# Kernel optimization log

Hardware: AMD Instinct MI355X
Metric: run time of the kernel (lower is better)

The kernel has to match this reference:

```python
import jax, jax.numpy as jnp
import numpy as np

N = 50000   # nodes
R = 4       # relation groups
E = 800000  # nnz per relation adjacency
ED = 200000 # decoded edges
H = 128     # hidden_dim
L = 64      # latent_dim
DH = 64     # decoder_hidden_dim


def setup_inputs() -> dict:
    key = jax.random.key(0)
    ks = iter(jax.random.split(key, 64))
    def nrm(shape, scale=1.0):
        return jax.random.normal(next(ks), shape, dtype=jnp.float32) * scale
    inp = {}
    inp["x_process"] = nrm((N, 62))
    inp["x_file"] = nrm((N, 37))
    inp["x_network"] = nrm((N, 37))
    def lin(prefix, din, dout):
        s = 1.0 / np.sqrt(din)
        inp[prefix + "_Ws"] = nrm((dout, din), s)
        inp[prefix + "_bs"] = nrm((dout,), s)
        inp[prefix + "_Wr"] = nrm((R, dout, din), s)
        inp[prefix + "_br"] = nrm((R, dout), s)
    lin("p1", 62, H); lin("p2", H, L)
    lin("f1", 37, H); lin("f2", H, L)
    lin("n1", 37, H); lin("n2", H, L)
    inp["gate_W"] = nrm((3, L), 1.0 / np.sqrt(L))
    inp["gate_b"] = nrm((3,), 0.1)
    inp["dec_W1"] = nrm((DH, 4 * L), 1.0 / np.sqrt(4 * L))
    inp["dec_b1"] = nrm((DH,), 0.1)
    inp["dec_W2"] = nrm((1, DH), 1.0 / np.sqrt(DH))
    inp["dec_b2"] = nrm((1,), 0.1)
    inp["adj_rows"] = jax.random.randint(next(ks), (R, E), 0, N, dtype=jnp.int32)
    inp["adj_cols"] = jax.random.randint(next(ks), (R, E), 0, N, dtype=jnp.int32)
    inp["adj_vals"] = jax.random.uniform(next(ks), (R, E), dtype=jnp.float32) * 0.1
    inp["edge_src"] = jax.random.randint(next(ks), (ED,), 0, N, dtype=jnp.int32)
    inp["edge_dst"] = jax.random.randint(next(ks), (ED,), 0, N, dtype=jnp.int32)
    return inp


def reference(x_process, x_file, x_network,
              p1_Ws, p1_bs, p1_Wr, p1_br, p2_Ws, p2_bs, p2_Wr, p2_br,
              f1_Ws, f1_bs, f1_Wr, f1_br, f2_Ws, f2_bs, f2_Wr, f2_br,
              n1_Ws, n1_bs, n1_Wr, n1_br, n2_Ws, n2_bs, n2_Wr, n2_br,
              gate_W, gate_b, dec_W1, dec_b1, dec_W2, dec_b2,
              adj_rows, adj_cols, adj_vals, edge_src, edge_dst):
    def spmm(rows, cols, vals, x):  # A @ x, A in COO: out[row] += val * x[col]
        return jax.ops.segment_sum(vals[:, None] * x[cols], rows, num_segments=N)

    def rgcn_layer(x, Ws, bs, Wr, br):
        out = x @ Ws.T + bs  # self_linear
        for r in range(R):
            out = out + spmm(adj_rows[r], adj_cols[r], adj_vals[r], x) @ Wr[r].T + br[r]
        return out / float(R + 1)

    def encoder(x, W1s, b1s, W1r, b1r, W2s, b2s, W2r, b2r):
        h = jax.nn.relu(rgcn_layer(x, W1s, b1s, W1r, b1r))
        # dropout p=0.0 / eval mode -> identity
        return rgcn_layer(h, W2s, b2s, W2r, b2r)

    z_p = encoder(x_process, p1_Ws, p1_bs, p1_Wr, p1_br, p2_Ws, p2_bs, p2_Wr, p2_br)
    z_f = encoder(x_file, f1_Ws, f1_bs, f1_Wr, f1_br, f2_Ws, f2_bs, f2_Wr, f2_br)
    z_n = encoder(x_network, n1_Ws, n1_bs, n1_Wr, n1_br, n2_Ws, n2_bs, n2_Wr, n2_br)

    # gated multi-view fusion: three Linear(latent,1) gates -> softmax over views
    scores = jnp.stack([z_p @ gate_W[0] + gate_b[0],
                        z_f @ gate_W[1] + gate_b[1],
                        z_n @ gate_W[2] + gate_b[2]], axis=1)  # [N, 3]
    alpha = jax.nn.softmax(scores, axis=1)
    z = alpha[:, 0:1] * z_p + alpha[:, 1:2] * z_f + alpha[:, 2:3] * z_n  # [N, L]

    # mlp edge decoder
    zs = z[edge_src]
    zd = z[edge_dst]
    feats = jnp.concatenate([zs, zd, zs * zd, jnp.abs(zs - zd)], axis=1)  # [ED, 4L]
    hid = jax.nn.relu(feats @ dec_W1.T + dec_b1)
    logits = (hid @ dec_W2.T + dec_b2)[:, 0]  # [ED]
    return logits
```

## Files before the change

### kernel.cpp

```cpp
#include <hip/hip_runtime.h>

#define N_NODES 50000
#define R_REL   4
#define E_NNZ   800000
#define ED_EDGES 200000
#define H_DIM   128
#define L_DIM   64

#define RN_TOTAL (R_REL * N_NODES)
#define ETOT     (R_REL * E_NNZ)

#define EPB   8192
#define NB    391
#define RBK   196
#define KBK   (R_REL * RBK)
#define HTOT  (KBK * NB)
#define SCB   300
#define MAXB  6144

#define WS_RP    0u
#define WS_HIST  800256u
#define WS_BSUM  2026496u
#define WS_BIAS3 2028544u
#define WS_CV    2030592u
#define WS_YALL  27630720u
#define WS_TMP   27630720u
#define WS_SF    53230720u
#define WS_SN    82830720u
#define WS_XALL  112430720u
#define WS_YSP   112430720u
#define WS_SP    131630720u
#define WS_HF    131630720u
#define WS_YSN   131630720u
#define WS_HN    157230720u
#define WS_HPR   188001536u
#define WS_YSF   188001536u
#define WS_Z     200801536u

__device__ __forceinline__ ushort f2bf(float f) {
    unsigned u = __float_as_uint(f);
    unsigned r = (u + 0x7fffu + ((u >> 16) & 1u)) >> 16;
    return (ushort)r;
}
__device__ __forceinline__ float bf2f(ushort u) {
    return __uint_as_float(((unsigned)u) << 16);
}

__global__ void cast_xall_kernel(const float* __restrict__ xp, const float* __restrict__ xf,
                                 const float* __restrict__ xn, ushort* __restrict__ xall) {
    int i = blockIdx.x * 256 + threadIdx.x;
    if (i >= N_NODES * 192) return;
    int node = i / 192, k = i - node * 192;
    float v = 0.f;
    if (k < 62) v = xp[node * 62 + k];
    else if (k >= 64 && k < 138) {
        int j = k - 64, d = j >> 1;
        v = (j & 1) ? xn[node * 37 + d] : xf[node * 37 + d];
    }
    xall[i] = f2bf(v);
}

__global__ void radix_hist_kernel(const int* __restrict__ rows, int* __restrict__ H) {
    __shared__ int hist[KBK];
    int blk = blockIdx.x, t = threadIdx.x;
    for (int i = t; i < KBK; i += 256) hist[i] = 0;
    __syncthreads();
    int base = blk * EPB;
    #pragma unroll 1
    for (int i = 0; i < EPB / 256; i++) {
        int g = base + i * 256 + t;
        if (g < ETOT) {
            int r = g / E_NNZ;
            atomicAdd(&hist[r * RBK + (rows[g] >> 8)], 1);
        }
    }
    __syncthreads();
    for (int i = t; i < KBK; i += 256) H[i * NB + blk] = hist[i];
}

__global__ void scan_part_kernel(const int* __restrict__ H, int* __restrict__ bsum) {
    __shared__ int red[256];
    int base = blockIdx.x * 1024, t = threadIdx.x;
    int s = 0;
    #pragma unroll
    for (int i = 0; i < 4; i++) {
        int idx = base + i * 256 + t;
        if (idx < HTOT) s += H[idx];
    }
    red[t] = s; __syncthreads();
    for (int d = 128; d > 0; d >>= 1) {
        if (t < d) red[t] += red[t + d];
        __syncthreads();
    }
    if (t == 0) bsum[blockIdx.x] = red[0];
}

__global__ void scan_bsum_kernel(int* __restrict__ bsum, int* __restrict__ rp) {
    __shared__ int sh[512];
    int t = threadIdx.x;
    int v = (t < SCB) ? bsum[t] : 0;
    sh[t] = v; __syncthreads();
    for (int d = 1; d < 512; d <<= 1) {
        int u = (t >= d) ? sh[t - d] : 0;
        __syncthreads();
        sh[t] += u;
        __syncthreads();
    }
    if (t < SCB) bsum[t] = sh[t] - v;
    if (t == 0) rp[RN_TOTAL] = ETOT;
}

__global__ void scan_final_kernel(int* __restrict__ H, const int* __restrict__ bsum) {
    __shared__ int sh[256];
    int base = blockIdx.x * 1024, t = threadIdx.x;
    int c[4]; int s = 0;
    #pragma unroll
    for (int i = 0; i < 4; i++) {
        int idx = base + t * 4 + i;
        c[i] = (idx < HTOT) ? H[idx] : 0;
        s += c[i];
    }
    sh[t] = s; __syncthreads();
    for (int d = 1; d < 256; d <<= 1) {
        int u = (t >= d) ? sh[t - d] : 0;
        __syncthreads();
        sh[t] += u;
        __syncthreads();
    }
    int off = bsum[blockIdx.x] + sh[t] - s;
    #pragma unroll
    for (int i = 0; i < 4; i++) {
        int idx = base + t * 4 + i;
        if (idx < HTOT) H[idx] = off;
        off += c[i];
    }
}

__global__ void radix_scatter_kernel(const int* __restrict__ rows, const int* __restrict__ cols,
                                     const float* __restrict__ vals, const int* __restrict__ H,
                                     int2* __restrict__ tmp) {
    __shared__ int cur[KBK];
    int blk = blockIdx.x, t = threadIdx.x;
    for (int i = t; i < KBK; i += 256) cur[i] = H[i * NB + blk];
    __syncthreads();
    int base = blk * EPB;
    #pragma unroll 1
    for (int i = 0; i < EPB / 256; i++) {
        int g = base + i * 256 + t;
        if (g < ETOT) {
            int r = g / E_NNZ;
            int row = rows[g];
            int b = r * RBK + (row >> 8);
            int p = atomicAdd(&cur[b], 1);
            tmp[p] = make_int2(cols[g] | ((row & 255) << 16), __float_as_int(vals[g]));
        }
    }
}

__launch_bounds__(256)
__global__ void bucket_sort_kernel(const int2* __restrict__ tmp, const int* __restrict__ H,
                                   int* __restrict__ rp, int2* __restrict__ cse) {
    __shared__ int hist[256];
    __shared__ int sc[256];
    __shared__ int cur[256];
    __shared__ int2 eb[MAXB];
    int b = blockIdx.x, t = threadIdx.x;
    int start = H[b * NB];
    int end = (b == KBK - 1) ? ETOT : H[(b + 1) * NB];
    int cnt = end - start;
    bool useLds = (cnt <= MAXB);
    hist[t] = 0;
    __syncthreads();
    for (int i = t; i < cnt; i += 256) {
        int2 e = tmp[start + i];
        if (useLds) eb[i] = e;
        atomicAdd(&hist[(e.x >> 16) & 255], 1);
    }
    __syncthreads();
    sc[t] = hist[t]; __syncthreads();
    for (int d = 1; d < 256; d <<= 1) {
        int v = (t >= d) ? sc[t - d] : 0;
        __syncthreads();
        sc[t] += v;
        __syncthreads();
    }
    int pref = sc[t] - hist[t];
    int r = b / RBK, rh = b - r * RBK;
    int grow = rh * 256 + t;
    if (grow < N_NODES) rp[r * N_NODES + grow] = start + pref;
    cur[t] = start + pref;
    __syncthreads();
    for (int i = t; i < cnt; i += 256) {
        int2 e = useLds ? eb[i] : tmp[start + i];
        int rl = (e.x >> 16) & 255;
        int p = atomicAdd(&cur[rl], 1);
        cse[p] = make_int2(e.x & 0xFFFF, e.y);
    }
}

__global__ void spmm1_all_kernel(const ushort* __restrict__ xall,
                                 const int* __restrict__ rp, const int2* __restrict__ cse,
                                 float* __restrict__ Sp, float* __restrict__ Sf,
                                 float* __restrict__ Sn) {
    int wave = threadIdx.x >> 6, lane = threadIdx.x & 63;
    int row = blockIdx.x * 4 + wave;
    if (row >= N_NODES) return;
    int h = lane >> 5, j = lane & 31;
    unsigned d0 = 2u * (unsigned)j;
    unsigned po = d0;
    unsigned fo = 64u + 2u * d0;
    for (int r = 0; r < R_REL; r++) {
        int e0 = rp[r * N_NODES + row], e1 = rp[r * N_NODES + row + 1];
        float ap0 = 0.f, ap1 = 0.f, af0 = 0.f, af1 = 0.f, an0 = 0.f, an1 = 0.f;
        int e = e0;
        for (; e + 8 <= e1; e += 8) {
            int2 qA = cse[e + h],     qB = cse[e + 2 + h];
            int2 qC = cse[e + 4 + h], qD = cse[e + 6 + h];
            unsigned bA = (unsigned)qA.x * 192u, bB = (unsigned)qB.x * 192u;
            unsigned bC = (unsigned)qC.x * 192u, bD = (unsigned)qD.x * 192u;
            ushort2 pA = *(const ushort2*)(xall + bA + po);
            ushort2 pB = *(const ushort2*)(xall + bB + po);
            ushort2 pC = *(const ushort2*)(xall + bC + po);
            ushort2 pD = *(const ushort2*)(xall + bD + po);
            ushort4 uA = *(const ushort4*)(xall + bA + fo);
            ushort4 uB = *(const ushort4*)(xall + bB + fo);
            ushort4 uC = *(const ushort4*)(xall + bC + fo);
            ushort4 uD = *(const ushort4*)(xall + bD + fo);
            float vA = __int_as_float(qA.y), vB = __int_as_float(qB.y);
            float vC = __int_as_float(qC.y), vD = __int_as_float(qD.y);
            ap0 += vA * bf2f(pA.x) + vB * bf2f(pB.x) + vC * bf2f(pC.x) + vD * bf2f(pD.x);
            ap1 += vA * bf2f(pA.y) + vB * bf2f(pB.y) + vC * bf2f(pC.y) + vD * bf2f(pD.y);
            af0 += vA * bf2f(uA.x) + vB * bf2f(uB.x) + vC * bf2f(uC.x) + vD * bf2f(uD.x);
            an0 += vA * bf2f(uA.y) + vB * bf2f(uB.y) + vC * bf2f(uC.y) + vD * bf2f(uD.y);
            af1 += vA * bf2f(uA.z) + vB * bf2f(uB.z) + vC * bf2f(uC.z) + vD * bf2f(uD.z);
            an1 += vA * bf2f(uA.w) + vB * bf2f(uB.w) + vC * bf2f(uC.w) + vD * bf2f(uD.w);
        }
        for (; e < e1; e += 2) {
            int idx = e + h;
            int2 q = cse[idx < e1 ? idx : e1 - 1];
            float v = (idx < e1) ? __int_as_float(q.y) : 0.f;
            unsigned b = (unsigned)q.x * 192u;
            ushort2 p = *(const ushort2*)(xall + b + po);
            ushort4 u = *(const ushort4*)(xall + b + fo);
            ap0 += v * bf2f(p.x); ap1 += v * bf2f(p.y);
            af0 += v * bf2f(u.x); an0 += v * bf2f(u.y);
            af1 += v * bf2f(u.z); an1 += v * bf2f(u.w);
        }
        ap0 += __shfl_xor(ap0, 32); ap1 += __shfl_xor(ap1, 32);
        af0 += __shfl_xor(af0, 32); af1 += __shfl_xor(af1, 32);
        an0 += __shfl_xor(an0, 32); an1 += __shfl_xor(an1, 32);
        if (h == 0) {
            int d = (int)d0;
            if (d < 62) *(float2*)(Sp + row * 248 + r * 62 + d) = make_float2(ap0, ap1);
            float* sfp = Sf + row * 148 + r * 37;
            float* snp = Sn + row * 148 + r * 37;
            if (d < 37) { sfp[d] = af0; snp[d] = an0; }
            if (d < 36) { sfp[d + 1] = af1; snp[d + 1] = an1; }
        }
    }
}

__launch_bounds__(256)
__global__ void gemm1_kernel(const float* __restrict__ x, const float* __restrict__ S,
                             const float* __restrict__ Ws, const float* __restrict__ bs,
                             const float* __restrict__ Wr, const float* __restrict__ br,
                             float* __restrict__ h, int din) {
    __shared__ float sA[64 * 63];
    __shared__ float sW[62 * 132];
    int t = threadIdx.x;
    int i0 = blockIdx.x * 64;
    int rg = t >> 5, cg = t & 31;
    float acc[8][4] = {};
    for (int s = 0; s < 5; s++) {
        const float* Aptr; int astride;
        if (s == 0) { Aptr = x; astride = din; }
        else        { Aptr = S + (s - 1) * din; astride = 4 * din; }
        const float* Wp = (s == 0) ? Ws : (Wr + (s - 1) * H_DIM * din);
        __syncthreads();
        for (int idx = t; idx < 64 * din; idx += 256) {
            int rr = idx / din, k = idx - rr * din;
            int grow = i0 + rr;
            sA[rr * 63 + k] = (grow < N_NODES) ? Aptr[grow * astride + k] : 0.f;
        }
        for (int idx = t; idx < H_DIM * din; idx += 256) {
            int j = idx / din, k = idx - j * din;
            sW[k * 132 + j] = Wp[j * din + k];
        }
        __syncthreads();
        for (int k = 0; k < din; k++) {
            float a[8];
            #pragma unroll
            for (int rr = 0; rr < 8; rr++) a[rr] = sA[(rg * 8 + rr) * 63 + k];
            float4 w = *(const float4*)&sW[k * 132 + cg * 4];
            #pragma unroll
            for (int rr = 0; rr < 8; rr++) {
                acc[rr][0] += a[rr] * w.x; acc[rr][1] += a[rr] * w.y;
                acc[rr][2] += a[rr] * w.z; acc[rr][3] += a[rr] * w.w;
            }
        }
    }
    int j0 = cg * 4;
    float btot[4];
    #pragma unroll
    for (int cc = 0; cc < 4; cc++) {
        float b = bs[j0 + cc];
        #pragma unroll
        for (int r = 0; r < R_REL; r++) b += br[r * H_DIM + j0 + cc];
        btot[cc] = b;
    }
    #pragma unroll
    for (int rr = 0; rr < 8; rr++) {
        int grow = i0 + rg * 8 + rr;
        if (grow < N_NODES) {
            float4 o;
            o.x = fmaxf((acc[rr][0] + btot[0]) * 0.2f, 0.f);
            o.y = fmaxf((acc[rr][1] + btot[1]) * 0.2f, 0.f);
            o.z = fmaxf((acc[rr][2] + btot[2]) * 0.2f, 0.f);
            o.w = fmaxf((acc[rr][3] + btot[3]) * 0.2f, 0.f);
            *(float4*)&h[grow * H_DIM + j0] = o;
        }
    }
}

__launch_bounds__(256)
__global__ void gemm2_kernel(const float* __restrict__ h, const float* __restrict__ Ws2,
                             const float* __restrict__ Wr2, float* __restrict__ Yself,
                             ushort* __restrict__ Yall, int view) {
    __shared__ float sA[128 * 65];
    __shared__ float sW[64 * 68];
    int t = threadIdx.x;
    int i0 = blockIdx.x * 128;
    int ct = blockIdx.y;
    int rg = t >> 4, cg = t & 15;
    const float* Wp = (ct == 0) ? Ws2 : (Wr2 + (ct - 1) * 64 * H_DIM);
    float acc[8][4] = {};
    for (int kc = 0; kc < 2; kc++) {
        __syncthreads();
        for (int idx = t; idx < 128 * 64; idx += 256) {
            int rr = idx >> 6, k = idx & 63;
            int grow = i0 + rr;
            sA[rr * 65 + k] = (grow < N_NODES) ? h[grow * H_DIM + kc * 64 + k] : 0.f;
        }
        for (int idx = t; idx < 64 * 64; idx += 256) {
            int j = idx >> 6, k = idx & 63;
            sW[k * 68 + j] = Wp[j * H_DIM + kc * 64 + k];
        }
        __syncthreads();
        for (int k = 0; k < 64; k++) {
            float a[8];
            #pragma unroll
            for (int rr = 0; rr < 8; rr++) a[rr] = sA[(rg * 8 + rr) * 65 + k];
            float4 w = *(const float4*)&sW[k * 68 + cg * 4];
            #pragma unroll
            for (int rr = 0; rr < 8; rr++) {
                acc[rr][0] += a[rr] * w.x; acc[rr][1] += a[rr] * w.y;
                acc[rr][2] += a[rr] * w.z; acc[rr][3] += a[rr] * w.w;
            }
        }
    }
    #pragma unroll
    for (int rr = 0; rr < 8; rr++) {
        int grow = i0 + rg * 8 + rr;
        if (grow < N_NODES) {
            if (ct == 0) {
                float4 o = make_float4(acc[rr][0], acc[rr][1], acc[rr][2], acc[rr][3]);
                *(float4*)&Yself[(size_t)grow * 64 + cg * 4] = o;
            } else {
                ushort4 o;
                o.x = f2bf(acc[rr][0]); o.y = f2bf(acc[rr][1]);
                o.z = f2bf(acc[rr][2]); o.w = f2bf(acc[rr][3]);
                *(ushort4*)&Yall[(size_t)grow * 768 + (ct - 1) * 192 + view * 64 + cg * 4] = o;
            }
        }
    }
}

__global__ void bias_prep_kernel(const float* __restrict__ pbs, const float* __restrict__ pbr,
                                 const float* __restrict__ fbs, const float* __restrict__ fbr,
                                 const float* __restrict__ nbs, const float* __restrict__ nbr,
                                 float* __restrict__ bias3) {
    int t = threadIdx.x;
    if (t >= 192) return;
    int view = t >> 6, d = t & 63;
    const float* bs = (view == 0) ? pbs : (view == 1) ? fbs : nbs;
    const float* br = (view == 0) ? pbr : (view == 1) ? fbr : nbr;
    float b = bs[d];
    #pragma unroll
    for (int r = 0; r < R_REL; r++) b += br[r * 64 + d];
    bias3[t] = b;
}

__launch_bounds__(256)
__global__ void spmm2z_all_kernel(const float* __restrict__ Ysp,
                                  const float* __restrict__ Ysf,
                                  const float* __restrict__ Ysn,
                                  const ushort* __restrict__ Yall,
                                  const int* __restrict__ rp, const int2* __restrict__ cse,
                                  const float* __restrict__ bias3,
                                  const float* __restrict__ gW, const float* __restrict__ gb,
                                  float* __restrict__ z) {
    int wave = threadIdx.x >> 6, lane = threadIdx.x & 63;
    int row = blockIdx.x * 4 + wave;
    if (row >= N_NODES) return;
    int h = lane >> 5, j = lane & 31;
    unsigned d0 = 2u * (unsigned)j;
    float aP0 = 0.f, aP1 = 0.f, aF0 = 0.f, aF1 = 0.f, aN0 = 0.f, aN1 = 0.f;
    for (int r = 0; r < R_REL; r++) {
        int e0 = rp[r * N_NODES + row], e1 = rp[r * N_NODES + row + 1];
        unsigned ofs = (unsigned)(r * 192) + d0;
        int e = e0;
        for (; e + 8 <= e1; e += 8) {
            int2 qA = cse[e + h],     qB = cse[e + 2 + h];
            int2 qC = cse[e + 4 + h], qD = cse[e + 6 + h];
            unsigned oA = (unsigned)qA.x * 768u + ofs;
            unsigned oB = (unsigned)qB.x * 768u + ofs;
            unsigned oC = (unsigned)qC.x * 768u + ofs;
            unsigned oD = (unsigned)qD.x * 768u + ofs;
            ushort2 pA = *(const ushort2*)(Yall + oA);
            ushort2 fA = *(const ushort2*)(Yall + oA + 64);
            ushort2 nA = *(const ushort2*)(Yall + oA + 128);
            ushort2 pB = *(const ushort2*)(Yall + oB);
            ushort2 fB = *(const ushort2*)(Yall + oB + 64);
            ushort2 nB = *(const ushort2*)(Yall + oB + 128);
            ushort2 pC = *(const ushort2*)(Yall + oC);
            ushort2 fC = *(const ushort2*)(Yall + oC + 64);
            ushort2 nC = *(const ushort2*)(Yall + oC + 128);
            ushort2 pD = *(const ushort2*)(Yall + oD);
            ushort2 fD = *(const ushort2*)(Yall + oD + 64);
            ushort2 nD = *(const ushort2*)(Yall + oD + 128);
            float vA = __int_as_float(qA.y), vB = __int_as_float(qB.y);
            float vC = __int_as_float(qC.y), vD = __int_as_float(qD.y);
            aP0 += vA * bf2f(pA.x) + vB * bf2f(pB.x) + vC * bf2f(pC.x) + vD * bf2f(pD.x);
            aP1 += vA * bf2f(pA.y) + vB * bf2f(pB.y) + vC * bf2f(pC.y) + vD * bf2f(pD.y);
            aF0 += vA * bf2f(fA.x) + vB * bf2f(fB.x) + vC * bf2f(fC.x) + vD * bf2f(fD.x);
            aF1 += vA * bf2f(fA.y) + vB * bf2f(fB.y) + vC * bf2f(fC.y) + vD * bf2f(fD.y);
            aN0 += vA * bf2f(nA.x) + vB * bf2f(nB.x) + vC * bf2f(nC.x) + vD * bf2f(nD.x);
            aN1 += vA * bf2f(nA.y) + vB * bf2f(nB.y) + vC * bf2f(nC.y) + vD * bf2f(nD.y);
        }
        for (; e < e1; e += 2) {
            int idx = e + h;
            int2 q = cse[idx < e1 ? idx : e1 - 1];
            float v = (idx < e1) ? __int_as_float(q.y) : 0.f;
            unsigned o = (unsigned)q.x * 768u + ofs;
            ushort2 p = *(const ushort2*)(Yall + o);
            ushort2 f = *(const ushort2*)(Yall + o + 64);
            ushort2 n = *(const ushort2*)(Yall + o + 128);
            aP0 += v * bf2f(p.x); aP1 += v * bf2f(p.y);
            aF0 += v * bf2f(f.x); aF1 += v * bf2f(f.y);
            aN0 += v * bf2f(n.x); aN1 += v * bf2f(n.y);
        }
    }
    aP0 += __shfl_xor(aP0, 32); aP1 += __shfl_xor(aP1, 32);
    aF0 += __shfl_xor(aF0, 32); aF1 += __shfl_xor(aF1, 32);
    aN0 += __shfl_xor(aN0, 32); aN1 += __shfl_xor(aN1, 32);
    size_t rb = (size_t)row * 64 + d0;
    float2 ysp = *(const float2*)(Ysp + rb);
    float2 ysf = *(const float2*)(Ysf + rb);
    float2 ysn = *(const float2*)(Ysn + rb);
    aP0 = (aP0 + ysp.x + bias3[d0]) * 0.2f;
    aP1 = (aP1 + ysp.y + bias3[d0 + 1]) * 0.2f;
    aF0 = (aF0 + ysf.x + bias3[64 + d0]) * 0.2f;
    aF1 = (aF1 + ysf.y + bias3[64 + d0 + 1]) * 0.2f;
    aN0 = (aN0 + ysn.x + bias3[128 + d0]) * 0.2f;
    aN1 = (aN1 + ysn.y + bias3[128 + d0 + 1]) * 0.2f;
    float sp = aP0 * gW[d0] + aP1 * gW[d0 + 1];
    float sf = aF0 * gW[64 + d0] + aF1 * gW[64 + d0 + 1];
    float sn = aN0 * gW[128 + d0] + aN1 * gW[128 + d0 + 1];
    #pragma unroll
    for (int d = 16; d >= 1; d >>= 1) {
        sp += __shfl_xor(sp, d);
        sf += __shfl_xor(sf, d);
        sn += __shfl_xor(sn, d);
    }
    sp += gb[0]; sf += gb[1]; sn += gb[2];
    float m = fmaxf(sp, fmaxf(sf, sn));
    float ep = __expf(sp - m), ef = __expf(sf - m), en = __expf(sn - m);
    float inv = 1.f / (ep + ef + en);
    if (h == 0) {
        float2 zo;
        zo.x = (ep * aP0 + ef * aF0 + en * aN0) * inv;
        zo.y = (ep * aP1 + ef * aF1 + en * aN1) * inv;
        *(float2*)(z + rb) = zo;
    }
}

__launch_bounds__(512)
__global__ void decoder6_kernel(const float* __restrict__ z, const int* __restrict__ esrc,
                                const int* __restrict__ edst, const float* __restrict__ w1,
                                const float* __restrict__ b1, const float* __restrict__ w2,
                                const float* __restrict__ b2, float* __restrict__ out) {
    __shared__ float sW1[16384];
    int t = threadIdx.x;
    for (int i = t; i < 4096; i += 512)
        ((float4*)sW1)[i] = ((const float4*)w1)[i];
    __syncthreads();
    int e = blockIdx.x * 512 + t;
    if (e >= ED_EDGES) return;
    int s = esrc[e], d = edst[e];
    const float4* zs = (const float4*)(z + (size_t)s * 64);
    const float4* zd = (const float4*)(z + (size_t)d * 64);
    float hid[64];
    #pragma unroll
    for (int j = 0; j < 64; j++) hid[j] = 0.f;
    #pragma unroll 1
    for (int kc = 0; kc < 16; kc++) {
        float4 a = zs[kc], b = zd[kc];
        float4 p, q;
        p.x = a.x * b.x; q.x = fabsf(a.x - b.x);
        p.y = a.y * b.y; q.y = fabsf(a.y - b.y);
        p.z = a.z * b.z; q.z = fabsf(a.z - b.z);
        p.w = a.w * b.w; q.w = fabsf(a.w - b.w);
        const float* wb0 = sW1 + kc * 4;
        #pragma unroll
        for (int j = 0; j < 64; j++) {
            const float* wr = wb0 + j * 256;
            float4 wa = *(const float4*)(wr);
            float4 wbv = *(const float4*)(wr + 64);
            float4 wc = *(const float4*)(wr + 128);
            float4 wd = *(const float4*)(wr + 192);
            hid[j] += a.x * wa.x + a.y * wa.y + a.z * wa.z + a.w * wa.w
                    + b.x * wbv.x + b.y * wbv.y + b.z * wbv.z + b.w * wbv.w
                    + p.x * wc.x + p.y * wc.y + p.z * wc.z + p.w * wc.w
                    + q.x * wd.x + q.y * wd.y + q.z * wd.z + q.w * wd.w;
        }
    }
    float lg = b2[0];
    #pragma unroll
    for (int j = 0; j < 64; j++)
        lg += fmaxf(hid[j] + b1[j], 0.f) * w2[j];
    out[e] = lg;
}

extern "C" void kernel_launch(void* const* d_in, const int* in_sizes, int n_in,
                              void* d_out, int out_size, void* d_ws, size_t ws_size,
                              hipStream_t stream) {
    const float* x_p = (const float*)d_in[0];
    const float* x_f = (const float*)d_in[1];
    const float* x_n = (const float*)d_in[2];
    const float* p1_Ws = (const float*)d_in[3];  const float* p1_bs = (const float*)d_in[4];
    const float* p1_Wr = (const float*)d_in[5];  const float* p1_br = (const float*)d_in[6];
    const float* p2_Ws = (const float*)d_in[7];  const float* p2_bs = (const float*)d_in[8];
    const float* p2_Wr = (const float*)d_in[9];  const float* p2_br = (const float*)d_in[10];
    const float* f1_Ws = (const float*)d_in[11]; const float* f1_bs = (const float*)d_in[12];
    const float* f1_Wr = (const float*)d_in[13]; const float* f1_br = (const float*)d_in[14];
    const float* f2_Ws = (const float*)d_in[15]; const float* f2_bs = (const float*)d_in[16];
    const float* f2_Wr = (const float*)d_in[17]; const float* f2_br = (const float*)d_in[18];
    const float* n1_Ws = (const float*)d_in[19]; const float* n1_bs = (const float*)d_in[20];
    const float* n1_Wr = (const float*)d_in[21]; const float* n1_br = (const float*)d_in[22];
    const float* n2_Ws = (const float*)d_in[23]; const float* n2_bs = (const float*)d_in[24];
    const float* n2_Wr = (const float*)d_in[25]; const float* n2_br = (const float*)d_in[26];
    const float* gate_W = (const float*)d_in[27]; const float* gate_b = (const float*)d_in[28];
    const float* dec_W1 = (const float*)d_in[29]; const float* dec_b1 = (const float*)d_in[30];
    const float* dec_W2 = (const float*)d_in[31]; const float* dec_b2 = (const float*)d_in[32];
    const int*   adj_rows = (const int*)d_in[33];
    const int*   adj_cols = (const int*)d_in[34];
    const float* adj_vals = (const float*)d_in[35];
    const int*   edge_src = (const int*)d_in[36];
    const int*   edge_dst = (const int*)d_in[37];

    char* ws = (char*)d_ws;
    int*    rp   = (int*)(ws + WS_RP);
    int*    H    = (int*)(ws + WS_HIST);
    int*    bsum = (int*)(ws + WS_BSUM);
    float*  bias3 = (float*)(ws + WS_BIAS3);
    int2*   cse  = (int2*)(ws + WS_CV);
    int2*   tmp  = (int2*)(ws + WS_TMP);
    ushort* xall = (ushort*)(ws + WS_XALL);
    ushort* Yall = (ushort*)(ws + WS_YALL);
    float*  S_p = (float*)(ws + WS_SP);
    float*  S_f = (float*)(ws + WS_SF);
    float*  S_n = (float*)(ws + WS_SN);
    float*  h_p = (float*)(ws + WS_HPR);
    float*  h_f = (float*)(ws + WS_HF);
    float*  h_n = (float*)(ws + WS_HN);
    float*  Ys_p = (float*)(ws + WS_YSP);
    float*  Ys_f = (float*)(ws + WS_YSF);
    float*  Ys_n = (float*)(ws + WS_YSN);
    float*  z    = (float*)(ws + WS_Z);
    float*  out  = (float*)d_out;

    cast_xall_kernel<<<(N_NODES * 192 + 255) / 256, 256, 0, stream>>>(x_p, x_f, x_n, xall);

    radix_hist_kernel<<<NB, 256, 0, stream>>>(adj_rows, H);
    scan_part_kernel<<<SCB, 256, 0, stream>>>(H, bsum);
    scan_bsum_kernel<<<1, 512, 0, stream>>>(bsum, rp);
    scan_final_kernel<<<SCB, 256, 0, stream>>>(H, bsum);
    radix_scatter_kernel<<<NB, 256, 0, stream>>>(adj_rows, adj_cols, adj_vals, H, tmp);
    bucket_sort_kernel<<<KBK, 256, 0, stream>>>(tmp, H, rp, cse);

    spmm1_all_kernel<<<N_NODES / 4, 256, 0, stream>>>(xall, rp, cse, S_p, S_f, S_n);

    int g1 = (N_NODES + 63) / 64;
    gemm1_kernel<<<g1, 256, 0, stream>>>(x_p, S_p, p1_Ws, p1_bs, p1_Wr, p1_br, h_p, 62);
    gemm1_kernel<<<g1, 256, 0, stream>>>(x_f, S_f, f1_Ws, f1_bs, f1_Wr, f1_br, h_f, 37);
    gemm1_kernel<<<g1, 256, 0, stream>>>(x_n, S_n, n1_Ws, n1_bs, n1_Wr, n1_br, h_n, 37);

    dim3 g2((N_NODES + 127) / 128, 5);
    gemm2_kernel<<<g2, 256, 0, stream>>>(h_p, p2_Ws, p2_Wr, Ys_p, Yall, 0);
    gemm2_kernel<<<g2, 256, 0, stream>>>(h_f, f2_Ws, f2_Wr, Ys_f, Yall, 1);
    gemm2_kernel<<<g2, 256, 0, stream>>>(h_n, n2_Ws, n2_Wr, Ys_n, Yall, 2);

    bias_prep_kernel<<<1, 192, 0, stream>>>(p2_bs, p2_br, f2_bs, f2_br, n2_bs, n2_br, bias3);
    spmm2z_all_kernel<<<N_NODES / 4, 256, 0, stream>>>(
        Ys_p, Ys_f, Ys_n, Yall, rp, cse, bias3, gate_W, gate_b, z);

    decoder6_kernel<<<(ED_EDGES + 511) / 512, 512, 0, stream>>>(
        z, edge_src, edge_dst, dec_W1, dec_b1, dec_W2, dec_b2, out);
}
```

Before: 1.436 ms.

## Split decoder hidden units across blocks and process two edges per thread

The decoder now splits the 64 hidden units into two halves along a second grid dimension. Each block stages only half of W1 in LDS (32 KB instead of 64 KB), and each thread computes two edges so every LDS weight load is reused twice. Per-half partial logits go to a workspace buffer and a new combine kernel sums them and adds the output bias. The intent is to cut LDS traffic per FLOP and raise occupancy. In exchange it adds an extra launch, a partial-sum round trip through global memory, and each z row is gathered twice (once per half).

```diff
diff --git a/kernel.cpp b/kernel.cpp
--- a/kernel.cpp
+++ b/kernel.cpp
@@ -25,6 +25,7 @@
 #define WS_CV    2030592u
 #define WS_YALL  27630720u
 #define WS_TMP   27630720u
+#define WS_PART  27630720u
 #define WS_SF    53230720u
 #define WS_SN    82830720u
 #define WS_XALL  112430720u
@@ -484,51 +485,84 @@
     }
 }
 
-__launch_bounds__(512)
-__global__ void decoder6_kernel(const float* __restrict__ z, const int* __restrict__ esrc,
+__launch_bounds__(256, 4)
+__global__ void decoder7_kernel(const float* __restrict__ z, const int* __restrict__ esrc,
                                 const int* __restrict__ edst, const float* __restrict__ w1,
                                 const float* __restrict__ b1, const float* __restrict__ w2,
-                                const float* __restrict__ b2, float* __restrict__ out) {
-    __shared__ float sW1[16384];
+                                float* __restrict__ part) {
+    __shared__ float sW1[8192];
     int t = threadIdx.x;
-    for (int i = t; i < 4096; i += 512)
-        ((float4*)sW1)[i] = ((const float4*)w1)[i];
+    int jh = blockIdx.y;
+    const float* w1h = w1 + jh * 32 * 256;
+    for (int i = t; i < 2048; i += 256)
+        ((float4*)sW1)[i] = ((const float4*)w1h)[i];
     __syncthreads();
-    int e = blockIdx.x * 512 + t;
-    if (e >= ED_EDGES) return;
-    int s = esrc[e], d = edst[e];
-    const float4* zs = (const float4*)(z + (size_t)s * 64);
-    const float4* zd = (const float4*)(z + (size_t)d * 64);
-    float hid[64];
-    #pragma unroll
-    for (int j = 0; j < 64; j++) hid[j] = 0.f;
+    int e1 = blockIdx.x * 512 + t;
+    int e2 = e1 + 256;
+    bool v2 = e2 < ED_EDGES;
+    if (e1 >= ED_EDGES) return;
+    int s1 = esrc[e1], d1 = edst[e1];
+    int s2 = v2 ? esrc[e2] : s1;
+    int d2 = v2 ? edst[e2] : d1;
+    const float4* zs1 = (const float4*)(z + (size_t)s1 * 64);
+    const float4* zd1 = (const float4*)(z + (size_t)d1 * 64);
+    const float4* zs2 = (const float4*)(z + (size_t)s2 * 64);
+    const float4* zd2 = (const float4*)(z + (size_t)d2 * 64);
+    float hid1[32], hid2[32];
+    #pragma unroll
+    for (int j = 0; j < 32; j++) { hid1[j] = 0.f; hid2[j] = 0.f; }
     #pragma unroll 1
     for (int kc = 0; kc < 16; kc++) {
-        float4 a = zs[kc], b = zd[kc];
-        float4 p, q;
-        p.x = a.x * b.x; q.x = fabsf(a.x - b.x);
-        p.y = a.y * b.y; q.y = fabsf(a.y - b.y);
-        p.z = a.z * b.z; q.z = fabsf(a.z - b.z);
-        p.w = a.w * b.w; q.w = fabsf(a.w - b.w);
+        float4 a1 = zs1[kc], b1v4 = zd1[kc];
+        float4 a2 = zs2[kc], b2v4 = zd2[kc];
+        float4 p1, q1, p2, q2;
+        p1.x = a1.x * b1v4.x; q1.x = fabsf(a1.x - b1v4.x);
+        p1.y = a1.y * b1v4.y; q1.y = fabsf(a1.y - b1v4.y);
+        p1.z = a1.z * b1v4.z; q1.z = fabsf(a1.z - b1v4.z);
+        p1.w = a1.w * b1v4.w; q1.w = fabsf(a1.w - b1v4.w);
+        p2.x = a2.x * b2v4.x; q2.x = fabsf(a2.x - b2v4.x);
+        p2.y = a2.y * b2v4.y; q2.y = fabsf(a2.y - b2v4.y);
+        p2.z = a2.z * b2v4.z; q2.z = fabsf(a2.z - b2v4.z);
+        p2.w = a2.w * b2v4.w; q2.w = fabsf(a2.w - b2v4.w);
         const float* wb0 = sW1 + kc * 4;
         #pragma unroll
-        for (int j = 0; j < 64; j++) {
+        for (int j = 0; j < 32; j++) {
             const float* wr = wb0 + j * 256;
             float4 wa = *(const float4*)(wr);
             float4 wbv = *(const float4*)(wr + 64);
             float4 wc = *(const float4*)(wr + 128);
             float4 wd = *(const float4*)(wr + 192);
-            hid[j] += a.x * wa.x + a.y * wa.y + a.z * wa.z + a.w * wa.w
-                    + b.x * wbv.x + b.y * wbv.y + b.z * wbv.z + b.w * wbv.w
-                    + p.x * wc.x + p.y * wc.y + p.z * wc.z + p.w * wc.w
-                    + q.x * wd.x + q.y * wd.y + q.z * wd.z + q.w * wd.w;
-        }
-    }
-    float lg = b2[0];
-    #pragma unroll
-    for (int j = 0; j < 64; j++)
-        lg += fmaxf(hid[j] + b1[j], 0.f) * w2[j];
-    out[e] = lg;
+            float s1ab = a1.x * wa.x + a1.y * wa.y + a1.z * wa.z + a1.w * wa.w
+                       + b1v4.x * wbv.x + b1v4.y * wbv.y + b1v4.z * wbv.z + b1v4.w * wbv.w;
+            float s1pq = p1.x * wc.x + p1.y * wc.y + p1.z * wc.z + p1.w * wc.w
+                       + q1.x * wd.x + q1.y * wd.y + q1.z * wd.z + q1.w * wd.w;
+            hid1[j] += s1ab + s1pq;
+            float s2ab = a2.x * wa.x + a2.y * wa.y + a2.z * wa.z + a2.w * wa.w
+                       + b2v4.x * wbv.x + b2v4.y * wbv.y + b2v4.z * wbv.z + b2v4.w * wbv.w;
+            float s2pq = p2.x * wc.x + p2.y * wc.y + p2.z * wc.z + p2.w * wc.w
+                       + q2.x * wd.x + q2.y * wd.y + q2.z * wd.z + q2.w * wd.w;
+            hid2[j] += s2ab + s2pq;
+        }
+    }
+    float lg1a = 0.f, lg1b = 0.f, lg2a = 0.f, lg2b = 0.f;
+    #pragma unroll
+    for (int j = 0; j < 32; j += 2) {
+        int gj = jh * 32 + j;
+        float bj0 = b1[gj], wj0 = w2[gj];
+        float bj1 = b1[gj + 1], wj1 = w2[gj + 1];
+        lg1a += fmaxf(hid1[j] + bj0, 0.f) * wj0;
+        lg1b += fmaxf(hid1[j + 1] + bj1, 0.f) * wj1;
+        lg2a += fmaxf(hid2[j] + bj0, 0.f) * wj0;
+        lg2b += fmaxf(hid2[j + 1] + bj1, 0.f) * wj1;
+    }
+    part[(size_t)jh * ED_EDGES + e1] = lg1a + lg1b;
+    if (v2) part[(size_t)jh * ED_EDGES + e2] = lg2a + lg2b;
+}
+
+__global__ void dec_combine_kernel(const float* __restrict__ part, const float* __restrict__ b2,
+                                   float* __restrict__ out) {
+    int e = blockIdx.x * 256 + threadIdx.x;
+    if (e < ED_EDGES) out[e] = part[e] + part[ED_EDGES + e] + b2[0];
 }
 
 extern "C" void kernel_launch(void* const* d_in, const int* in_sizes, int n_in,
@@ -577,6 +611,7 @@
     float*  Ys_f = (float*)(ws + WS_YSF);
     float*  Ys_n = (float*)(ws + WS_YSN);
     float*  z    = (float*)(ws + WS_Z);
+    float*  part = (float*)(ws + WS_PART);
     float*  out  = (float*)d_out;
 
     cast_xall_kernel<<<(N_NODES * 192 + 255) / 256, 256, 0, stream>>>(x_p, x_f, x_n, xall);
@@ -604,6 +639,8 @@
     spmm2z_all_kernel<<<N_NODES / 4, 256, 0, stream>>>(
         Ys_p, Ys_f, Ys_n, Yall, rp, cse, bias3, gate_W, gate_b, z);
 
-    decoder6_kernel<<<(ED_EDGES + 511) / 512, 512, 0, stream>>>(
-        z, edge_src, edge_dst, dec_W1, dec_b1, dec_W2, dec_b2, out);
-}
+    dim3 gd((ED_EDGES + 511) / 512, 2);
+    decoder7_kernel<<<gd, 256, 0, stream>>>(
+        z, edge_src, edge_dst, dec_W1, dec_b1, dec_W2, part);
+    dec_combine_kernel<<<(ED_EDGES + 255) / 256, 256, 0, stream>>>(part, dec_b2, out);
+}
```

Measured after the change: 4.567 ms. +218.1%, slower.

## Precompute per-node decoder projections for src/dst halves of first layer

Applied to the files above, without the earlier changes.

Splits the decoder's first linear layer: the zs and zd blocks of W1 are applied once per node in a new GEMM kernel, producing U=z·W1a^T+b1 and V=z·W1b^T. These are stored with z in an interleaved per-node buffer. The edge kernel then only computes the zs*zd and |zs-zd| terms and adds the gathered U[src] and V[dst], halving per-edge FLOPs and the shared-memory weight footprint. The cost is an extra N×64×128 GEMM, a larger 192-float per-node buffer that is gathered randomly, and reuse of the workspace region that previously held Yall/tmp.

```diff
diff --git a/kernel.cpp b/kernel.cpp
--- a/kernel.cpp
+++ b/kernel.cpp
@@ -25,6 +25,7 @@
 #define WS_CV    2030592u
 #define WS_YALL  27630720u
 #define WS_TMP   27630720u
+#define WS_UVZ   27630720u
 #define WS_SF    53230720u
 #define WS_SN    82830720u
 #define WS_XALL  112430720u
@@ -484,27 +485,85 @@
     }
 }
 
-__launch_bounds__(512)
-__global__ void decoder6_kernel(const float* __restrict__ z, const int* __restrict__ esrc,
+__launch_bounds__(256)
+__global__ void uvgemm_kernel(const float* __restrict__ z, const float* __restrict__ w1,
+                              const float* __restrict__ b1, float* __restrict__ uvz) {
+    __shared__ float sA[128 * 65];
+    __shared__ float sW[64 * 68];
+    int t = threadIdx.x;
+    int i0 = blockIdx.x * 128;
+    int ct = blockIdx.y;
+    int rg = t >> 4, cg = t & 15;
+    for (int idx = t; idx < 128 * 64; idx += 256) {
+        int rr = idx >> 6, k = idx & 63;
+        int grow = i0 + rr;
+        sA[rr * 65 + k] = (grow < N_NODES) ? z[(size_t)grow * 64 + k] : 0.f;
+    }
+    for (int idx = t; idx < 64 * 64; idx += 256) {
+        int j = idx >> 6, k = idx & 63;
+        sW[k * 68 + j] = w1[j * 256 + ct * 64 + k];
+    }
+    __syncthreads();
+    float acc[8][4] = {};
+    for (int k = 0; k < 64; k++) {
+        float a[8];
+        #pragma unroll
+        for (int rr = 0; rr < 8; rr++) a[rr] = sA[(rg * 8 + rr) * 65 + k];
+        float4 w = *(const float4*)&sW[k * 68 + cg * 4];
+        #pragma unroll
+        for (int rr = 0; rr < 8; rr++) {
+            acc[rr][0] += a[rr] * w.x; acc[rr][1] += a[rr] * w.y;
+            acc[rr][2] += a[rr] * w.z; acc[rr][3] += a[rr] * w.w;
+        }
+    }
+    int j0 = cg * 4;
+    float4 bv = make_float4(0.f, 0.f, 0.f, 0.f);
+    if (ct == 0) {
+        bv.x = b1[j0]; bv.y = b1[j0 + 1]; bv.z = b1[j0 + 2]; bv.w = b1[j0 + 3];
+    }
+    unsigned voff = (ct == 0) ? 0u : 128u;
+    #pragma unroll
+    for (int rr = 0; rr < 8; rr++) {
+        int grow = i0 + rg * 8 + rr;
+        if (grow < N_NODES) {
+            float4 o = make_float4(acc[rr][0] + bv.x, acc[rr][1] + bv.y,
+                                   acc[rr][2] + bv.z, acc[rr][3] + bv.w);
+            *(float4*)&uvz[(size_t)grow * 192 + voff + j0] = o;
+        }
+    }
+    if (ct == 0) {
+        for (int idx = t; idx < 128 * 64; idx += 256) {
+            int rr = idx >> 6, k = idx & 63;
+            int grow = i0 + rr;
+            if (grow < N_NODES) uvz[(size_t)grow * 192 + 64 + k] = sA[rr * 65 + k];
+        }
+    }
+}
+
+__launch_bounds__(256)
+__global__ void decoder9_kernel(const float* __restrict__ uvz, const int* __restrict__ esrc,
                                 const int* __restrict__ edst, const float* __restrict__ w1,
-                                const float* __restrict__ b1, const float* __restrict__ w2,
-                                const float* __restrict__ b2, float* __restrict__ out) {
-    __shared__ float sW1[16384];
+                                const float* __restrict__ w2, const float* __restrict__ b2,
+                                float* __restrict__ out) {
+    __shared__ float sW1[8192];
     int t = threadIdx.x;
-    for (int i = t; i < 4096; i += 512)
-        ((float4*)sW1)[i] = ((const float4*)w1)[i];
-    __syncthreads();
-    int e = blockIdx.x * 512 + t;
+    for (int i = t; i < 2048; i += 256) {
+        int j = i >> 5, c = i & 31;
+        ((float4*)sW1)[i] = *(const float4*)(w1 + j * 256 + 128 + c * 4);
+    }
+    __syncthreads();
+    int e = blockIdx.x * 256 + t;
     if (e >= ED_EDGES) return;
     int s = esrc[e], d = edst[e];
-    const float4* zs = (const float4*)(z + (size_t)s * 64);
-    const float4* zd = (const float4*)(z + (size_t)d * 64);
+    const float4* su = (const float4*)(uvz + (size_t)s * 192);
+    const float4* dv = (const float4*)(uvz + (size_t)d * 192 + 64);
     float hid[64];
     #pragma unroll
     for (int j = 0; j < 64; j++) hid[j] = 0.f;
     #pragma unroll 1
     for (int kc = 0; kc < 16; kc++) {
-        float4 a = zs[kc], b = zd[kc];
+        float4 a = su[16 + kc];
+        float4 b = dv[kc];
         float4 p, q;
         p.x = a.x * b.x; q.x = fabsf(a.x - b.x);
         p.y = a.y * b.y; q.y = fabsf(a.y - b.y);
@@ -513,21 +572,25 @@
         const float* wb0 = sW1 + kc * 4;
         #pragma unroll
         for (int j = 0; j < 64; j++) {
-            const float* wr = wb0 + j * 256;
-            float4 wa = *(const float4*)(wr);
-            float4 wbv = *(const float4*)(wr + 64);
-            float4 wc = *(const float4*)(wr + 128);
-            float4 wd = *(const float4*)(wr + 192);
-            hid[j] += a.x * wa.x + a.y * wa.y + a.z * wa.z + a.w * wa.w
-                    + b.x * wbv.x + b.y * wbv.y + b.z * wbv.z + b.w * wbv.w
-                    + p.x * wc.x + p.y * wc.y + p.z * wc.z + p.w * wc.w
+            const float* wr = wb0 + j * 128;
+            float4 wc = *(const float4*)(wr);
+            float4 wd = *(const float4*)(wr + 64);
+            hid[j] += p.x * wc.x + p.y * wc.y + p.z * wc.z + p.w * wc.w
                     + q.x * wd.x + q.y * wd.y + q.z * wd.z + q.w * wd.w;
         }
     }
     float lg = b2[0];
     #pragma unroll
-    for (int j = 0; j < 64; j++)
-        lg += fmaxf(hid[j] + b1[j], 0.f) * w2[j];
+    for (int jj = 0; jj < 16; jj++) {
+        float4 u = su[jj];
+        float4 v = dv[16 + jj];
+        int gj = jj * 4;
+        float w0 = w2[gj], w1v = w2[gj + 1], w2v = w2[gj + 2], w3v = w2[gj + 3];
+        lg += fmaxf(hid[gj]     + u.x + v.x, 0.f) * w0
+            + fmaxf(hid[gj + 1] + u.y + v.y, 0.f) * w1v
+            + fmaxf(hid[gj + 2] + u.z + v.z, 0.f) * w2v
+            + fmaxf(hid[gj + 3] + u.w + v.w, 0.f) * w3v;
+    }
     out[e] = lg;
 }
 
@@ -577,6 +640,7 @@
     float*  Ys_f = (float*)(ws + WS_YSF);
     float*  Ys_n = (float*)(ws + WS_YSN);
     float*  z    = (float*)(ws + WS_Z);
+    float*  uvz  = (float*)(ws + WS_UVZ);
     float*  out  = (float*)d_out;
 
     cast_xall_kernel<<<(N_NODES * 192 + 255) / 256, 256, 0, stream>>>(x_p, x_f, x_n, xall);
@@ -604,6 +668,9 @@
     spmm2z_all_kernel<<<N_NODES / 4, 256, 0, stream>>>(
         Ys_p, Ys_f, Ys_n, Yall, rp, cse, bias3, gate_W, gate_b, z);
 
-    decoder6_kernel<<<(ED_EDGES + 511) / 512, 512, 0, stream>>>(
-        z, edge_src, edge_dst, dec_W1, dec_b1, dec_W2, dec_b2, out);
-}
+    dim3 guv((N_NODES + 127) / 128, 2);
+    uvgemm_kernel<<<guv, 256, 0, stream>>>(z, dec_W1, dec_b1, uvz);
+
+    decoder9_kernel<<<(ED_EDGES + 255) / 256, 256, 0, stream>>>(
+        uvz, edge_src, edge_dst, dec_W1, dec_W2, dec_b2, out);
+}
```

Measured after the change: 1.381 ms. 3.8% less time.
